# Kernel optimization log

Hardware: AMD Instinct MI355X
Metric: run time of the kernel (lower is better)

## Reference

```python
import jax, jax.numpy as jnp
import numpy as np

B, IN_CH, N, DIM, PH, HID, K = 4, 128, 2048, 256, 64, 1024, 16
EPS = 1e-5


def conv1(x, w, b):
    # 1x1 Conv1d: x (B,C,N), w (O,C) -> (B,O,N)
    return jnp.einsum('oc,bcn->bon', w, x) + b[None, :, None]


def conv2(x, w, b):
    # 1x1 Conv2d: x (B,C,N,K), w (O,C) -> (B,O,N,K)
    return jnp.einsum('oc,bcnk->bonk', w, x) + b[None, :, None, None]


def bn2(x, g, beta, mean, var):
    # eval-mode BatchNorm2d over channel dim of (B,C,N,K)
    scale = g * jax.lax.rsqrt(var + EPS)
    return x * scale[None, :, None, None] + (beta - mean * scale)[None, :, None, None]


def query_knn(pos, k):
    # pos: (B,3,N). Returns (B,N,K) indices of k nearest neighbors (incl. self).
    p = jnp.transpose(pos, (0, 2, 1))                     # (B,N,3)
    sq = jnp.sum(p * p, axis=-1)                          # (B,N)
    dist = sq[:, :, None] + sq[:, None, :] - 2.0 * jnp.einsum('bnc,bmc->bnm', p, p)
    _, idx = jax.lax.top_k(-dist, k)                      # smallest distances first
    return idx


def group(feat, idx):
    # feat: (B,C,N), idx: (B,N,K) -> (B,C,N,K) where out[b,c,i,k]=feat[b,c,idx[b,i,k]]
    b, c, n = feat.shape
    k = idx.shape[-1]
    ib = jnp.broadcast_to(idx.reshape(b, 1, n * k), (b, c, n * k))
    return jnp.take_along_axis(feat, ib, axis=2).reshape(b, c, n, k)


def setup_inputs() -> dict:
    key = jax.random.key(0)
    ks = jax.random.split(key, 12)
    s = 0.02
    return {
        'x': jax.random.normal(ks[0], (B, IN_CH, N), jnp.float32),
        'pos': jax.random.normal(ks[1], (B, 3, N), jnp.float32),
        'ls_w': jax.random.normal(ks[2], (DIM, IN_CH), jnp.float32) * s,
        'ls_b': jnp.zeros((DIM,), jnp.float32),
        'kw': jax.random.normal(ks[3], (DIM, DIM), jnp.float32) * s,
        'kb': jnp.zeros((DIM,), jnp.float32),
        'qw': jax.random.normal(ks[4], (DIM, DIM), jnp.float32) * s,
        'qb': jnp.zeros((DIM,), jnp.float32),
        'vw': jax.random.normal(ks[5], (DIM, DIM), jnp.float32) * s,
        'vb': jnp.zeros((DIM,), jnp.float32),
        'pw1': jax.random.normal(ks[6], (PH, 3), jnp.float32) * s,
        'pb1': jnp.zeros((PH,), jnp.float32),
        'pg': jnp.ones((PH,), jnp.float32),
        'pbeta': jnp.zeros((PH,), jnp.float32),
        'pmean': jnp.zeros((PH,), jnp.float32),
        'pvar': jnp.ones((PH,), jnp.float32),
        'pw2': jax.random.normal(ks[7], (DIM, PH), jnp.float32) * s,
        'pb2': jnp.zeros((DIM,), jnp.float32),
        'aw1': jax.random.normal(ks[8], (HID, DIM), jnp.float32) * s,
        'ab1': jnp.zeros((HID,), jnp.float32),
        'ag': jnp.ones((HID,), jnp.float32),
        'abeta': jnp.zeros((HID,), jnp.float32),
        'amean': jnp.zeros((HID,), jnp.float32),
        'avar': jnp.ones((HID,), jnp.float32),
        'aw2': jax.random.normal(ks[9], (DIM, HID), jnp.float32) * s,
        'ab2': jnp.zeros((DIM,), jnp.float32),
        'lw': jax.random.normal(ks[10], (IN_CH, DIM), jnp.float32) * s,
        'lb': jnp.zeros((IN_CH,), jnp.float32),
    }


def reference(x, pos, ls_w, ls_b, kw, kb, qw, qb, vw, vb,
              pw1, pb1, pg, pbeta, pmean, pvar, pw2, pb2,
              aw1, ab1, ag, abeta, amean, avar, aw2, ab2, lw, lb):
    identity = x
    h = conv1(x, ls_w, ls_b)                              # (B,DIM,N)
    idx = query_knn(pos, K)                               # (B,N,K) int32
    key_f = group(conv1(h, kw, kb), idx)                  # (B,DIM,N,K)
    value = conv1(h, vw, vb)                              # (B,DIM,N)
    query = conv1(h, qw, qb)                              # (B,DIM,N)
    qk_rel = query[:, :, :, None] - key_f                 # (B,DIM,N,K)
    pos_rel = pos[:, :, :, None] - group(pos, idx)        # (B,3,N,K)
    pe = conv2(jax.nn.relu(bn2(conv2(pos_rel, pw1, pb1), pg, pbeta, pmean, pvar)), pw2, pb2)
    attn = conv2(jax.nn.relu(bn2(conv2(qk_rel + pe, aw1, ab1), ag, abeta, amean, avar)), aw2, ab2)
    attn = jax.nn.softmax(attn, axis=-1)                  # softmax over K
    val_g = group(value, idx) + pe                        # (B,DIM,N,K)
    agg = jnp.sum(attn * val_g, axis=-1)                  # (B,DIM,N)
    y = conv1(agg, lw, lb)                                # (B,IN_CH,N)
    return y + identity
```

## Files before the change

### kernel.cpp

```cpp
#include <hip/hip_runtime.h>
#include <hip/hip_bf16.h>
#include <math.h>

#define B_    4
#define CIN   128
#define NPTS  2048
#define DIM   256
#define PH    64
#define HIDN  1024
#define KNN_  16
#define BN    (B_*NPTS)
#define CC    (BN*KNN_)
#define EPS_  1e-5f

typedef __bf16 bf16;
typedef __bf16 bf16x8 __attribute__((ext_vector_type(8)));
typedef __bf16 bf16x4 __attribute__((ext_vector_type(4)));
typedef float  f32x4  __attribute__((ext_vector_type(4)));

__global__ __launch_bounds__(256) void prep_kernel(
    const float* __restrict__ ls_w, const float* __restrict__ kw,
    const float* __restrict__ qw,   const float* __restrict__ vw,
    const float* __restrict__ pw2,  const float* __restrict__ aw1,
    const float* __restrict__ aw2,  const float* __restrict__ lw,
    const float* __restrict__ pb1,  const float* __restrict__ pg,
    const float* __restrict__ pbeta,const float* __restrict__ pmean,
    const float* __restrict__ pvar,
    const float* __restrict__ ab1,  const float* __restrict__ ag,
    const float* __restrict__ abeta,const float* __restrict__ amean,
    const float* __restrict__ avar,
    const float* __restrict__ qb,   const float* __restrict__ kb,
    const float* __restrict__ vb,
    bf16* ls_wb, bf16* qkvw, bf16* pw2b, bf16* aw1b, bf16* aw2b, bf16* lwb,
    float* pe_scale, float* pe_shift, float* at_scale, float* at_shift,
    float* qkvb)
{
  long e = (long)blockIdx.x * 256 + threadIdx.x;
  if (e < 32768)  { ls_wb[e] = (bf16)ls_w[e]; return; } e -= 32768;
  if (e < 65536)  { qkvw[e]          = (bf16)qw[e]; return; } e -= 65536;
  if (e < 65536)  { qkvw[65536 + e]  = (bf16)kw[e]; return; } e -= 65536;
  if (e < 65536)  { qkvw[131072 + e] = (bf16)vw[e]; return; } e -= 65536;
  if (e < 16384)  { pw2b[e]  = (bf16)pw2[e];  return; } e -= 16384;
  if (e < 262144) { aw1b[e]  = (bf16)aw1[e];  return; } e -= 262144;
  if (e < 262144) { aw2b[e]  = (bf16)aw2[e];  return; } e -= 262144;
  if (e < 32768)  { lwb[e]   = (bf16)lw[e];   return; } e -= 32768;
  if (e < 64) {
    float sc = pg[e] * rsqrtf(pvar[e] + EPS_);
    pe_scale[e] = sc;
    pe_shift[e] = sc * pb1[e] + pbeta[e] - pmean[e] * sc;
    return;
  } e -= 64;
  if (e < 1024) {
    float sc = ag[e] * rsqrtf(avar[e] + EPS_);
    at_scale[e] = sc;
    at_shift[e] = sc * ab1[e] + abeta[e] - amean[e] * sc;
    return;
  } e -= 1024;
  if (e < 768) {
    qkvb[e] = (e < 256) ? qb[e] : (e < 512) ? kb[e - 256] : vb[e - 512];
  }
}

__global__ __launch_bounds__(256) void transpose_x_kernel(
    const float* __restrict__ x, bf16* __restrict__ xT)
{
  __shared__ float tile[CIN][65];
  const int tid = threadIdx.x;
  const int b = blockIdx.x >> 5;
  const int n0 = (blockIdx.x & 31) * 64;
  const float* xb = x + (long)b * CIN * NPTS;
#pragma unroll
  for (int it = 0; it < 32; ++it) {
    int row = it * 4 + (tid >> 6);
    int n = tid & 63;
    tile[row][n] = xb[(long)row * NPTS + n0 + n];
  }
  __syncthreads();
#pragma unroll
  for (int it = 0; it < 4; ++it) {
    int c = it * 256 + tid;
    int n = c >> 4;
    int ch0 = (c & 15) * 8;
    bf16x8 v;
#pragma unroll
    for (int j = 0; j < 8; ++j) v[j] = (bf16)tile[ch0 + j][n];
    *(bf16x8*)&xT[((long)b * NPTS + n0 + n) * CIN + ch0] = v;
  }
}

__global__ __launch_bounds__(256) void knn_kernel(
    const float* __restrict__ pos, int* __restrict__ idx_out)
{
  __shared__ float px[NPTS], py[NPTS], pz[NPTS];
  const int tid = threadIdx.x;
  const int lane = tid & 63, wave = tid >> 6;
  const int q = blockIdx.x * 4 + wave;
  const int b = q >> 11;
  const int n = q & (NPTS - 1);
  const float* p = pos + (long)b * 3 * NPTS;
  for (int j = tid; j < NPTS; j += 256) {
    px[j] = p[j]; py[j] = p[NPTS + j]; pz[j] = p[2 * NPTS + j];
  }
  __syncthreads();
  float qx = px[n], qy = py[n], qz = pz[n];
  float qs = qx * qx + qy * qy + qz * qz;
  float d[32];
#pragma unroll
  for (int j = 0; j < 32; ++j) {
    int pt = j * 64 + lane;
    float x = px[pt], y = py[pt], z = pz[pt];
    float s2 = x * x + y * y + z * z;
    float dt = qx * x + qy * y + qz * z;
    d[j] = qs + s2 - 2.f * dt;
  }
  for (int r = 0; r < KNN_; ++r) {
    float bv = 1e30f; int bj = 0;
#pragma unroll
    for (int j = 0; j < 32; ++j)
      if (d[j] < bv) { bv = d[j]; bj = j; }
    int bi = bj * 64 + lane;
#pragma unroll
    for (int off = 32; off >= 1; off >>= 1) {
      float ov = __shfl_xor(bv, off);
      int   oi = __shfl_xor(bi, off);
      if (ov < bv || (ov == bv && oi < bi)) { bv = ov; bi = oi; }
    }
    if (lane == 0) idx_out[(long)q * KNN_ + r] = bi;
#pragma unroll
    for (int j = 0; j < 32; ++j)
      if (bi == j * 64 + lane) d[j] = 1e30f;
  }
}

template<int KD, bool OBF16>
__global__ __launch_bounds__(256) void gemmT_kernel(
    const bf16* __restrict__ inT, const bf16* __restrict__ Wb,
    const float* __restrict__ bias, void* __restrict__ outp, int O)
{
  const int tid = threadIdx.x;
  const int lane = tid & 63, wave = tid >> 6;
  const int row16 = lane & 15, grp = lane >> 4;
  const long i0 = (long)blockIdx.x * 64 + (wave & 1) * 32;
  const long o0 = (long)blockIdx.y * 64 + (wave >> 1) * 32;
  f32x4 acc[2][2] = {};
  const bf16* a0p = inT + (i0 + row16) * KD + grp * 8;
  const bf16* a1p = a0p + 16 * KD;
  const bf16* b0p = Wb + (o0 + row16) * KD + grp * 8;
  const bf16* b1p = b0p + 16 * KD;
#pragma unroll
  for (int ks = 0; ks < KD / 32; ++ks) {
    bf16x8 a0 = *(const bf16x8*)(a0p + ks * 32);
    bf16x8 a1 = *(const bf16x8*)(a1p + ks * 32);
    bf16x8 b0 = *(const bf16x8*)(b0p + ks * 32);
    bf16x8 b1 = *(const bf16x8*)(b1p + ks * 32);
    acc[0][0] = __builtin_amdgcn_mfma_f32_16x16x32_bf16(a0, b0, acc[0][0], 0, 0, 0);
    acc[0][1] = __builtin_amdgcn_mfma_f32_16x16x32_bf16(a0, b1, acc[0][1], 0, 0, 0);
    acc[1][0] = __builtin_amdgcn_mfma_f32_16x16x32_bf16(a1, b0, acc[1][0], 0, 0, 0);
    acc[1][1] = __builtin_amdgcn_mfma_f32_16x16x32_bf16(a1, b1, acc[1][1], 0, 0, 0);
  }
#pragma unroll
  for (int ot = 0; ot < 2; ++ot) {
    long o = o0 + ot * 16 + row16;
    float bv = bias[o];
#pragma unroll
    for (int it = 0; it < 2; ++it) {
#pragma unroll
      for (int r = 0; r < 4; ++r) {
        long i = i0 + it * 16 + grp * 4 + r;
        float v = acc[it][ot][r] + bv;
        if (OBF16) ((bf16*)outp)[i * O + o] = (bf16)v;
        else       ((float*)outp)[i * O + o] = v;
      }
    }
  }
}

__global__ __launch_bounds__(512, 4) void attn_fused_kernel(
    const bf16* __restrict__ qkvT, const float* __restrict__ pos,
    const int* __restrict__ idx, const float* __restrict__ pw1,
    const float* __restrict__ pe_scale, const float* __restrict__ pe_shift,
    const bf16* __restrict__ pw2b, const float* __restrict__ pb2,
    const bf16* __restrict__ aw1b, const bf16* __restrict__ aw2b,
    const float* __restrict__ at_scale, const float* __restrict__ at_shift,
    const float* __restrict__ ab2, bf16* __restrict__ aggT)
{
  __shared__ __align__(16) bf16 u_lds[64][264];
  __shared__ __align__(16) bf16 tbuf[64 * 136];
  __shared__ float rel_lds[64][4];
  __shared__ int   idx_lds[64];
  bf16 (*t_lds)[136]  = (bf16(*)[136])tbuf;
  bf16 (*hid_lds)[72] = (bf16(*)[72])tbuf;

  const int tid = threadIdx.x;
  const int lane = tid & 63, wave = tid >> 6;
  const int row16 = lane & 15, grp = lane >> 4;
  const long c0 = (long)blockIdx.x * 64;
  const int bn0 = blockIdx.x * 4;
  const int b = bn0 >> 11;
  const float* pB = pos + (long)b * 3 * NPTS;
  const int os = wave * 32;

  if (tid < 64) {
    int nb = idx[c0 + tid];
    idx_lds[tid] = nb;
    int n = (bn0 + (tid >> 4)) & (NPTS - 1);
    rel_lds[tid][0] = pB[n] - pB[nb];
    rel_lds[tid][1] = pB[NPTS + n] - pB[NPTS + nb];
    rel_lds[tid][2] = pB[2 * NPTS + n] - pB[2 * NPTS + nb];
  }
#pragma unroll
  for (int it = 0; it < 4; ++it) {
    int id = it * 512 + tid;
    int col = id >> 5, ch16 = id & 31;
    int nb = idx[c0 + col];
    *(bf16x8*)&u_lds[col][ch16 * 8] =
        *(const bf16x8*)(qkvT + ((long)b * NPTS + nb) * 768 + 256 + ch16 * 8);
  }
  __syncthreads();

  {
    int c = tid & 63, jq = tid >> 6;
    float rx = rel_lds[c][0], ry = rel_lds[c][1], rz = rel_lds[c][2];
#pragma unroll
    for (int jj = 0; jj < 8; ++jj) {
      int j = jq * 8 + jj;
      float v = pw1[j * 3] * rx + pw1[j * 3 + 1] * ry + pw1[j * 3 + 2] * rz;
      v = pe_scale[j] * v + pe_shift[j];
      hid_lds[c][j] = (bf16)fmaxf(v, 0.f);
    }
  }
  __syncthreads();

  f32x4 accpe[4][2] = {};
#pragma unroll
  for (int ks = 0; ks < 2; ++ks) {
    bf16x8 ah[4];
#pragma unroll
    for (int ct = 0; ct < 4; ++ct)
      ah[ct] = *(const bf16x8*)&hid_lds[ct * 16 + row16][ks * 32 + grp * 8];
#pragma unroll
    for (int ot = 0; ot < 2; ++ot) {
      bf16x8 bw = *(const bf16x8*)(pw2b + (long)(os + ot * 16 + row16) * PH + ks * 32 + grp * 8);
#pragma unroll
      for (int ct = 0; ct < 4; ++ct)
        accpe[ct][ot] = __builtin_amdgcn_mfma_f32_16x16x32_bf16(ah[ct], bw, accpe[ct][ot], 0, 0, 0);
    }
  }

  bf16x4 pe_bf[4][2];
#pragma unroll
  for (int ot = 0; ot < 2; ++ot) {
    int o = os + ot * 16 + row16;
    float pb2v = pb2[o];
#pragma unroll
    for (int ct = 0; ct < 4; ++ct) {
      float qv = (float)qkvT[(long)(bn0 + ct) * 768 + o];
#pragma unroll
      for (int r = 0; r < 4; ++r) {
        int c = ct * 16 + grp * 4 + r;
        float pev = accpe[ct][ot][r] + pb2v;
        float kv = (float)u_lds[c][o];
        u_lds[c][o] = (bf16)(qv - kv + pev);
        pe_bf[ct][ot][r] = (bf16)pev;
      }
    }
  }
  __syncthreads();

  const int hs = wave * 32;
  const int hs16 = wave * 16;
  f32x4 acc2[4][2] = {};
  for (int jc = 0; jc < 8; ++jc) {
    const int hg = jc * 128 + hs16;
    f32x4 acc1[4] = {};
#pragma unroll
    for (int ks = 0; ks < 8; ++ks) {
      bf16x8 bu[4];
#pragma unroll
      for (int ct = 0; ct < 4; ++ct)
        bu[ct] = *(const bf16x8*)&u_lds[ct * 16 + row16][ks * 32 + grp * 8];
      bf16x8 aw = *(const bf16x8*)(aw1b + (long)(hg + row16) * DIM + ks * 32 + grp * 8);
#pragma unroll
      for (int ct = 0; ct < 4; ++ct)
        acc1[ct] = __builtin_amdgcn_mfma_f32_16x16x32_bf16(aw, bu[ct], acc1[ct], 0, 0, 0);
    }
    {
      f32x4 sc4 = *(const f32x4*)&at_scale[hg + grp * 4];
      f32x4 sh4 = *(const f32x4*)&at_shift[hg + grp * 4];
#pragma unroll
      for (int ct = 0; ct < 4; ++ct) {
        bf16x4 pk;
#pragma unroll
        for (int r = 0; r < 4; ++r) {
          float v = sc4[r] * acc1[ct][r] + sh4[r];
          pk[r] = (bf16)fmaxf(v, 0.f);
        }
        *(bf16x4*)&t_lds[ct * 16 + row16][hs16 + grp * 4] = pk;
      }
    }
    __syncthreads();
#pragma unroll
    for (int ks2 = 0; ks2 < 4; ++ks2) {
      bf16x8 a2[4], b2;
#pragma unroll
      for (int ct = 0; ct < 4; ++ct)
        a2[ct] = *(const bf16x8*)&t_lds[ct * 16 + row16][ks2 * 32 + grp * 8];
#pragma unroll
      for (int ot = 0; ot < 2; ++ot) {
        b2 = *(const bf16x8*)(aw2b + (long)(os + ot * 16 + row16) * HIDN + jc * 128 + ks2 * 32 + grp * 8);
#pragma unroll
        for (int ct = 0; ct < 4; ++ct)
          acc2[ct][ot] = __builtin_amdgcn_mfma_f32_16x16x32_bf16(a2[ct], b2, acc2[ct][ot], 0, 0, 0);
      }
    }
    __syncthreads();
  }

#pragma unroll
  for (int ct = 0; ct < 4; ++ct) {
#pragma unroll
    for (int ot = 0; ot < 2; ++ot) {
      int o = os + ot * 16 + row16;
      float ab = ab2[o];
      float l[4];
      float m = -1e30f;
#pragma unroll
      for (int r = 0; r < 4; ++r) {
        l[r] = acc2[ct][ot][r] + ab;
        m = fmaxf(m, l[r]);
      }
      m = fmaxf(m, __shfl_xor(m, 16));
      m = fmaxf(m, __shfl_xor(m, 32));
      float s = 0.f;
#pragma unroll
      for (int r = 0; r < 4; ++r) { l[r] = __expf(l[r] - m); s += l[r]; }
      s += __shfl_xor(s, 16);
      s += __shfl_xor(s, 32);
      float inv = 1.f / s;
      float agg = 0.f;
#pragma unroll
      for (int r = 0; r < 4; ++r) {
        int c = ct * 16 + grp * 4 + r;
        int nb = idx_lds[c];
        float vv = (float)qkvT[((long)b * NPTS + nb) * 768 + 512 + o];
        agg += l[r] * (vv + (float)pe_bf[ct][ot][r]);
      }
      agg *= inv;
      agg += __shfl_xor(agg, 16);
      agg += __shfl_xor(agg, 32);
      if (grp == 0) aggT[(long)(bn0 + ct) * DIM + o] = (bf16)agg;
    }
  }
}

__global__ __launch_bounds__(256) void final_kernel(
    const bf16* __restrict__ aggT, const bf16* __restrict__ lwb,
    const float* __restrict__ lb, const float* __restrict__ x,
    float* __restrict__ out)
{
  const int tid = threadIdx.x;
  const int lane = tid & 63, wave = tid >> 6;
  const int row16 = lane & 15, grp = lane >> 4;
  const long i0 = (long)blockIdx.x * 64 + (wave & 1) * 32;
  const int o0 = blockIdx.y * 64 + (wave >> 1) * 32;
  f32x4 acc[2][2] = {};
  const bf16* a0p = aggT + (i0 + row16) * DIM + grp * 8;
  const bf16* a1p = a0p + 16 * DIM;
  const bf16* b0p = lwb + (long)(o0 + row16) * DIM + grp * 8;
  const bf16* b1p = b0p + 16 * DIM;
#pragma unroll
  for (int ks = 0; ks < 8; ++ks) {
    bf16x8 a0 = *(const bf16x8*)(a0p + ks * 32);
    bf16x8 a1 = *(const bf16x8*)(a1p + ks * 32);
    bf16x8 b0 = *(const bf16x8*)(b0p + ks * 32);
    bf16x8 b1 = *(const bf16x8*)(b1p + ks * 32);
    acc[0][0] = __builtin_amdgcn_mfma_f32_16x16x32_bf16(a0, b0, acc[0][0], 0, 0, 0);
    acc[0][1] = __builtin_amdgcn_mfma_f32_16x16x32_bf16(a0, b1, acc[0][1], 0, 0, 0);
    acc[1][0] = __builtin_amdgcn_mfma_f32_16x16x32_bf16(a1, b0, acc[1][0], 0, 0, 0);
    acc[1][1] = __builtin_amdgcn_mfma_f32_16x16x32_bf16(a1, b1, acc[1][1], 0, 0, 0);
  }
#pragma unroll
  for (int ot = 0; ot < 2; ++ot) {
    int o = o0 + ot * 16 + row16;
    float bv = lb[o];
#pragma unroll
    for (int it = 0; it < 2; ++it) {
#pragma unroll
      for (int r = 0; r < 4; ++r) {
        long i = i0 + it * 16 + grp * 4 + r;
        int bb = (int)(i >> 11);
        int n = (int)(i & (NPTS - 1));
        long off = ((long)bb * CIN + o) * NPTS + n;
        out[off] = acc[it][ot][r] + bv + x[off];
      }
    }
  }
}

extern "C" void kernel_launch(void* const* d_in, const int* in_sizes, int n_in,
                              void* d_out, int out_size, void* d_ws, size_t ws_size,
                              hipStream_t stream)
{
  const float* x     = (const float*)d_in[0];
  const float* pos   = (const float*)d_in[1];
  const float* ls_w  = (const float*)d_in[2];
  const float* ls_b  = (const float*)d_in[3];
  const float* kw    = (const float*)d_in[4];
  const float* kb    = (const float*)d_in[5];
  const float* qw    = (const float*)d_in[6];
  const float* qb    = (const float*)d_in[7];
  const float* vw    = (const float*)d_in[8];
  const float* vb    = (const float*)d_in[9];
  const float* pw1   = (const float*)d_in[10];
  const float* pb1   = (const float*)d_in[11];
  const float* pg    = (const float*)d_in[12];
  const float* pbeta = (const float*)d_in[13];
  const float* pmean = (const float*)d_in[14];
  const float* pvar  = (const float*)d_in[15];
  const float* pw2   = (const float*)d_in[16];
  const float* pb2   = (const float*)d_in[17];
  const float* aw1   = (const float*)d_in[18];
  const float* ab1   = (const float*)d_in[19];
  const float* ag    = (const float*)d_in[20];
  const float* abeta = (const float*)d_in[21];
  const float* amean = (const float*)d_in[22];
  const float* avar  = (const float*)d_in[23];
  const float* aw2   = (const float*)d_in[24];
  const float* ab2   = (const float*)d_in[25];
  const float* lw    = (const float*)d_in[26];
  const float* lb    = (const float*)d_in[27];

  char* ws = (char*)d_ws;
  size_t off = 0;
  auto alloc = [&](size_t bytes) -> void* {
    void* p = ws + off;
    off = (off + bytes + 255) & ~(size_t)255;
    return p;
  };

  bf16* ls_wb = (bf16*)alloc(32768 * 2);
  bf16* qkvw  = (bf16*)alloc(196608 * 2);
  bf16* pw2b  = (bf16*)alloc(16384 * 2);
  bf16* aw1b  = (bf16*)alloc(262144 * 2);
  bf16* aw2b  = (bf16*)alloc(262144 * 2);
  bf16* lwb   = (bf16*)alloc(32768 * 2);
  float* pe_scale = (float*)alloc(64 * 4);
  float* pe_shift = (float*)alloc(64 * 4);
  float* at_scale = (float*)alloc(1024 * 4);
  float* at_shift = (float*)alloc(1024 * 4);
  float* qkvb = (float*)alloc(768 * 4);
  int*  idx  = (int*)alloc((size_t)CC * 4);
  bf16* xT   = (bf16*)alloc((size_t)BN * CIN * 2);
  bf16* hT   = (bf16*)alloc((size_t)BN * DIM * 2);
  bf16* qkvT = (bf16*)alloc((size_t)BN * 768 * 2);
  bf16* aggT = (bf16*)alloc((size_t)BN * DIM * 2);

  prep_kernel<<<dim3((804672 + 255) / 256), 256, 0, stream>>>(
      ls_w, kw, qw, vw, pw2, aw1, aw2, lw,
      pb1, pg, pbeta, pmean, pvar, ab1, ag, abeta, amean, avar,
      qb, kb, vb,
      ls_wb, qkvw, pw2b, aw1b, aw2b, lwb,
      pe_scale, pe_shift, at_scale, at_shift, qkvb);

  transpose_x_kernel<<<dim3(B_ * 32), 256, 0, stream>>>(x, xT);

  knn_kernel<<<dim3(BN / 4), 256, 0, stream>>>(pos, idx);

  gemmT_kernel<128, true><<<dim3(BN / 64, DIM / 64), 256, 0, stream>>>(xT, ls_wb, ls_b, hT, DIM);

  gemmT_kernel<256, true><<<dim3(BN / 64, 768 / 64), 256, 0, stream>>>(hT, qkvw, qkvb, qkvT, 768);

  attn_fused_kernel<<<dim3(CC / 64), 512, 0, stream>>>(
      qkvT, pos, idx, pw1, pe_scale, pe_shift, pw2b, pb2,
      aw1b, aw2b, at_scale, at_shift, ab2, aggT);

  final_kernel<<<dim3(BN / 64, CIN / 64), 256, 0, stream>>>(aggT, lwb, lb, x, (float*)d_out);
}
```

Measured before the change: 477.9 us.

## XOR-swizzle attention LDS tiles, drop padding, raise occupancy hint

Replaces the padded shared-memory arrays in the fused attention kernel with unpadded buffers using an XOR swizzle on 8-element blocks. The aim is to avoid LDS bank conflicts on the MFMA operand reads while shrinking the LDS footprint. The relative-position scratch now lives inside the reusable tbuf region, and neighbor indices are re-read from global memory instead of LDS. The launch bound's occupancy hint rises from 4 to 6, which tightens the register budget and risks spills.

```diff
diff --git a/kernel.cpp b/kernel.cpp
--- a/kernel.cpp
+++ b/kernel.cpp
@@ -175,7 +175,7 @@
   }
 }
 
-__global__ __launch_bounds__(512, 4) void attn_fused_kernel(
+__global__ __launch_bounds__(512, 6) void attn_fused_kernel(
     const bf16* __restrict__ qkvT, const float* __restrict__ pos,
     const int* __restrict__ idx, const float* __restrict__ pw1,
     const float* __restrict__ pe_scale, const float* __restrict__ pe_shift,
@@ -184,16 +184,16 @@
     const float* __restrict__ at_scale, const float* __restrict__ at_shift,
     const float* __restrict__ ab2, bf16* __restrict__ aggT)
 {
-  __shared__ __align__(16) bf16 u_lds[64][264];
-  __shared__ __align__(16) bf16 tbuf[64 * 136];
-  __shared__ float rel_lds[64][4];
-  __shared__ int   idx_lds[64];
-  bf16 (*t_lds)[136]  = (bf16(*)[136])tbuf;
-  bf16 (*hid_lds)[72] = (bf16(*)[72])tbuf;
+  __shared__ __align__(16) bf16 u_lds[64 * 256];
+  __shared__ __align__(16) bf16 tbuf[64 * 128];
+  bf16* t_lds   = tbuf;
+  bf16* hid_lds = tbuf;
+  float (*rel4)[4] = (float(*)[4])(tbuf + 6144);
 
   const int tid = threadIdx.x;
   const int lane = tid & 63, wave = tid >> 6;
   const int row16 = lane & 15, grp = lane >> 4;
+  const int r7 = row16 & 7;
   const long c0 = (long)blockIdx.x * 64;
   const int bn0 = blockIdx.x * 4;
   const int b = bn0 >> 11;
@@ -202,32 +202,33 @@
 
   if (tid < 64) {
     int nb = idx[c0 + tid];
-    idx_lds[tid] = nb;
     int n = (bn0 + (tid >> 4)) & (NPTS - 1);
-    rel_lds[tid][0] = pB[n] - pB[nb];
-    rel_lds[tid][1] = pB[NPTS + n] - pB[NPTS + nb];
-    rel_lds[tid][2] = pB[2 * NPTS + n] - pB[2 * NPTS + nb];
+    rel4[tid][0] = pB[n] - pB[nb];
+    rel4[tid][1] = pB[NPTS + n] - pB[NPTS + nb];
+    rel4[tid][2] = pB[2 * NPTS + n] - pB[2 * NPTS + nb];
   }
 #pragma unroll
   for (int it = 0; it < 4; ++it) {
     int id = it * 512 + tid;
     int col = id >> 5, ch16 = id & 31;
     int nb = idx[c0 + col];
-    *(bf16x8*)&u_lds[col][ch16 * 8] =
+    *(bf16x8*)&u_lds[col * 256 + ((ch16 ^ (col & 7)) << 3)] =
         *(const bf16x8*)(qkvT + ((long)b * NPTS + nb) * 768 + 256 + ch16 * 8);
   }
   __syncthreads();
 
   {
     int c = tid & 63, jq = tid >> 6;
-    float rx = rel_lds[c][0], ry = rel_lds[c][1], rz = rel_lds[c][2];
+    float rx = rel4[c][0], ry = rel4[c][1], rz = rel4[c][2];
+    bf16x8 pk8;
 #pragma unroll
     for (int jj = 0; jj < 8; ++jj) {
       int j = jq * 8 + jj;
       float v = pw1[j * 3] * rx + pw1[j * 3 + 1] * ry + pw1[j * 3 + 2] * rz;
       v = pe_scale[j] * v + pe_shift[j];
-      hid_lds[c][j] = (bf16)fmaxf(v, 0.f);
-    }
+      pk8[jj] = (bf16)fmaxf(v, 0.f);
+    }
+    *(bf16x8*)&hid_lds[c * 64 + ((jq ^ (c & 7)) << 3)] = pk8;
   }
   __syncthreads();
 
@@ -237,7 +238,7 @@
     bf16x8 ah[4];
 #pragma unroll
     for (int ct = 0; ct < 4; ++ct)
-      ah[ct] = *(const bf16x8*)&hid_lds[ct * 16 + row16][ks * 32 + grp * 8];
+      ah[ct] = *(const bf16x8*)&hid_lds[(ct * 16 + row16) * 64 + (((ks * 4 + grp) ^ r7) << 3)];
 #pragma unroll
     for (int ot = 0; ot < 2; ++ot) {
       bf16x8 bw = *(const bf16x8*)(pw2b + (long)(os + ot * 16 + row16) * PH + ks * 32 + grp * 8);
@@ -258,16 +259,16 @@
 #pragma unroll
       for (int r = 0; r < 4; ++r) {
         int c = ct * 16 + grp * 4 + r;
+        int ua = c * 256 + (((o >> 3) ^ (c & 7)) << 3) + (o & 7);
         float pev = accpe[ct][ot][r] + pb2v;
-        float kv = (float)u_lds[c][o];
-        u_lds[c][o] = (bf16)(qv - kv + pev);
+        float kv = (float)u_lds[ua];
+        u_lds[ua] = (bf16)(qv - kv + pev);
         pe_bf[ct][ot][r] = (bf16)pev;
       }
     }
   }
   __syncthreads();
 
-  const int hs = wave * 32;
   const int hs16 = wave * 16;
   f32x4 acc2[4][2] = {};
   for (int jc = 0; jc < 8; ++jc) {
@@ -276,9 +277,10 @@
 #pragma unroll
     for (int ks = 0; ks < 8; ++ks) {
       bf16x8 bu[4];
+      const int ublk = ((ks * 4 + grp) ^ r7) << 3;
 #pragma unroll
       for (int ct = 0; ct < 4; ++ct)
-        bu[ct] = *(const bf16x8*)&u_lds[ct * 16 + row16][ks * 32 + grp * 8];
+        bu[ct] = *(const bf16x8*)&u_lds[(ct * 16 + row16) * 256 + ublk];
       bf16x8 aw = *(const bf16x8*)(aw1b + (long)(hg + row16) * DIM + ks * 32 + grp * 8);
 #pragma unroll
       for (int ct = 0; ct < 4; ++ct)
@@ -295,7 +297,9 @@
           float v = sc4[r] * acc1[ct][r] + sh4[r];
           pk[r] = (bf16)fmaxf(v, 0.f);
         }
-        *(bf16x4*)&t_lds[ct * 16 + row16][hs16 + grp * 4] = pk;
+        int trow = ct * 16 + row16;
+        int tblk = (wave * 2 + (grp >> 1)) ^ (trow & 7);
+        *(bf16x4*)&t_lds[trow * 128 + (tblk << 3) + ((grp & 1) << 2)] = pk;
       }
     }
     __syncthreads();
@@ -304,7 +308,7 @@
       bf16x8 a2[4], b2;
 #pragma unroll
       for (int ct = 0; ct < 4; ++ct)
-        a2[ct] = *(const bf16x8*)&t_lds[ct * 16 + row16][ks2 * 32 + grp * 8];
+        a2[ct] = *(const bf16x8*)&t_lds[(ct * 16 + row16) * 128 + (((ks2 * 4 + grp) ^ r7) << 3)];
 #pragma unroll
       for (int ot = 0; ot < 2; ++ot) {
         b2 = *(const bf16x8*)(aw2b + (long)(os + ot * 16 + row16) * HIDN + jc * 128 + ks2 * 32 + grp * 8);
@@ -341,7 +345,7 @@
 #pragma unroll
       for (int r = 0; r < 4; ++r) {
         int c = ct * 16 + grp * 4 + r;
-        int nb = idx_lds[c];
+        int nb = idx[c0 + c];
         float vv = (float)qkvT[((long)b * NPTS + nb) * 768 + 512 + o];
         agg += l[r] * (vv + (float)pe_bf[ct][ot][r]);
       }
```

Result: slower. 542.4 us (+13.5%).

## Fold linear-stem conv into QKV weights and merge setup kernels into one launch

Applied to the files above, without the earlier changes.

The 1x1 stem conv (ls_w) is folded algebraically into the Q/K/V projection weights and biases, computed on device, so the QKV GEMM runs directly on the transposed input with K=128. This removes the intermediate h tensor and one GEMM. The prep, transpose, kNN and weight-fold work are combined into a single launch partitioned by block index, which cuts launch count. The folded weights are rounded to bf16 after an fp32 product, which changes numerics slightly, and the fold blocks run a naive serial 256-step loop per output row.

```diff
diff --git a/kernel.cpp b/kernel.cpp
--- a/kernel.cpp
+++ b/kernel.cpp
@@ -18,9 +18,20 @@
 typedef __bf16 bf16x4 __attribute__((ext_vector_type(4)));
 typedef float  f32x4  __attribute__((ext_vector_type(4)));
 
-__global__ __launch_bounds__(256) void prep_kernel(
-    const float* __restrict__ ls_w, const float* __restrict__ kw,
-    const float* __restrict__ qw,   const float* __restrict__ vw,
+#define KNN_END   2048
+#define PREP_CNT  2245
+#define PREP_END  (KNN_END + PREP_CNT)
+#define TR_END    (PREP_END + 128)
+#define FOLD_END  (TR_END + 192)
+
+__global__ __launch_bounds__(256) void combo_kernel(
+    const float* __restrict__ pos, int* __restrict__ idx_out,
+    const float* __restrict__ x, bf16* __restrict__ xT,
+    const float* __restrict__ ls_w, const float* __restrict__ ls_b,
+    const float* __restrict__ qw, const float* __restrict__ kw,
+    const float* __restrict__ vw,
+    const float* __restrict__ qb, const float* __restrict__ kb,
+    const float* __restrict__ vb,
     const float* __restrict__ pw2,  const float* __restrict__ aw1,
     const float* __restrict__ aw2,  const float* __restrict__ lw,
     const float* __restrict__ pb1,  const float* __restrict__ pg,
@@ -29,106 +40,122 @@
     const float* __restrict__ ab1,  const float* __restrict__ ag,
     const float* __restrict__ abeta,const float* __restrict__ amean,
     const float* __restrict__ avar,
-    const float* __restrict__ qb,   const float* __restrict__ kb,
-    const float* __restrict__ vb,
-    bf16* ls_wb, bf16* qkvw, bf16* pw2b, bf16* aw1b, bf16* aw2b, bf16* lwb,
+    bf16* pw2b, bf16* aw1b, bf16* aw2b, bf16* lwb,
     float* pe_scale, float* pe_shift, float* at_scale, float* at_shift,
-    float* qkvb)
+    bf16* wfold, float* bfold)
 {
-  long e = (long)blockIdx.x * 256 + threadIdx.x;
-  if (e < 32768)  { ls_wb[e] = (bf16)ls_w[e]; return; } e -= 32768;
-  if (e < 65536)  { qkvw[e]          = (bf16)qw[e]; return; } e -= 65536;
-  if (e < 65536)  { qkvw[65536 + e]  = (bf16)kw[e]; return; } e -= 65536;
-  if (e < 65536)  { qkvw[131072 + e] = (bf16)vw[e]; return; } e -= 65536;
-  if (e < 16384)  { pw2b[e]  = (bf16)pw2[e];  return; } e -= 16384;
-  if (e < 262144) { aw1b[e]  = (bf16)aw1[e];  return; } e -= 262144;
-  if (e < 262144) { aw2b[e]  = (bf16)aw2[e];  return; } e -= 262144;
-  if (e < 32768)  { lwb[e]   = (bf16)lw[e];   return; } e -= 32768;
-  if (e < 64) {
-    float sc = pg[e] * rsqrtf(pvar[e] + EPS_);
-    pe_scale[e] = sc;
-    pe_shift[e] = sc * pb1[e] + pbeta[e] - pmean[e] * sc;
+  __shared__ __align__(16) char smem[33280];
+  const int bid = blockIdx.x;
+  const int tid = threadIdx.x;
+
+  if (bid < KNN_END) {
+    float* px = (float*)smem;
+    float* py = px + NPTS;
+    float* pz = py + NPTS;
+    const int lane = tid & 63, wave = tid >> 6;
+    const int q = bid * 4 + wave;
+    const int b = q >> 11;
+    const int n = q & (NPTS - 1);
+    const float* p = pos + (long)b * 3 * NPTS;
+    for (int j = tid; j < NPTS; j += 256) {
+      px[j] = p[j]; py[j] = p[NPTS + j]; pz[j] = p[2 * NPTS + j];
+    }
+    __syncthreads();
+    float qx = px[n], qy = py[n], qz = pz[n];
+    float qs = qx * qx + qy * qy + qz * qz;
+    float d[32];
+#pragma unroll
+    for (int j = 0; j < 32; ++j) {
+      int pt = j * 64 + lane;
+      float xx = px[pt], yy = py[pt], zz = pz[pt];
+      float s2 = xx * xx + yy * yy + zz * zz;
+      float dt = qx * xx + qy * yy + qz * zz;
+      d[j] = qs + s2 - 2.f * dt;
+    }
+    for (int r = 0; r < KNN_; ++r) {
+      float bv = 1e30f; int bj = 0;
+#pragma unroll
+      for (int j = 0; j < 32; ++j)
+        if (d[j] < bv) { bv = d[j]; bj = j; }
+      int bi = bj * 64 + lane;
+#pragma unroll
+      for (int off = 32; off >= 1; off >>= 1) {
+        float ov = __shfl_xor(bv, off);
+        int   oi = __shfl_xor(bi, off);
+        if (ov < bv || (ov == bv && oi < bi)) { bv = ov; bi = oi; }
+      }
+      if (lane == 0) idx_out[(long)q * KNN_ + r] = bi;
+#pragma unroll
+      for (int j = 0; j < 32; ++j)
+        if (bi == j * 64 + lane) d[j] = 1e30f;
+    }
     return;
-  } e -= 64;
-  if (e < 1024) {
-    float sc = ag[e] * rsqrtf(avar[e] + EPS_);
-    at_scale[e] = sc;
-    at_shift[e] = sc * ab1[e] + abeta[e] - amean[e] * sc;
+  }
+
+  if (bid < PREP_END) {
+    long e = (long)(bid - KNN_END) * 256 + tid;
+    if (e < 16384)  { pw2b[e] = (bf16)pw2[e]; return; } e -= 16384;
+    if (e < 262144) { aw1b[e] = (bf16)aw1[e]; return; } e -= 262144;
+    if (e < 262144) { aw2b[e] = (bf16)aw2[e]; return; } e -= 262144;
+    if (e < 32768)  { lwb[e]  = (bf16)lw[e];  return; } e -= 32768;
+    if (e < 64) {
+      float sc = pg[e] * rsqrtf(pvar[e] + EPS_);
+      pe_scale[e] = sc;
+      pe_shift[e] = sc * pb1[e] + pbeta[e] - pmean[e] * sc;
+      return;
+    } e -= 64;
+    if (e < 1024) {
+      float sc = ag[e] * rsqrtf(avar[e] + EPS_);
+      at_scale[e] = sc;
+      at_shift[e] = sc * ab1[e] + abeta[e] - amean[e] * sc;
+    }
     return;
-  } e -= 1024;
-  if (e < 768) {
-    qkvb[e] = (e < 256) ? qb[e] : (e < 512) ? kb[e - 256] : vb[e - 512];
-  }
-}
-
-__global__ __launch_bounds__(256) void transpose_x_kernel(
-    const float* __restrict__ x, bf16* __restrict__ xT)
-{
-  __shared__ float tile[CIN][65];
-  const int tid = threadIdx.x;
-  const int b = blockIdx.x >> 5;
-  const int n0 = (blockIdx.x & 31) * 64;
-  const float* xb = x + (long)b * CIN * NPTS;
-#pragma unroll
-  for (int it = 0; it < 32; ++it) {
-    int row = it * 4 + (tid >> 6);
-    int n = tid & 63;
-    tile[row][n] = xb[(long)row * NPTS + n0 + n];
-  }
-  __syncthreads();
-#pragma unroll
-  for (int it = 0; it < 4; ++it) {
-    int c = it * 256 + tid;
-    int n = c >> 4;
-    int ch0 = (c & 15) * 8;
-    bf16x8 v;
-#pragma unroll
-    for (int j = 0; j < 8; ++j) v[j] = (bf16)tile[ch0 + j][n];
-    *(bf16x8*)&xT[((long)b * NPTS + n0 + n) * CIN + ch0] = v;
-  }
-}
-
-__global__ __launch_bounds__(256) void knn_kernel(
-    const float* __restrict__ pos, int* __restrict__ idx_out)
-{
-  __shared__ float px[NPTS], py[NPTS], pz[NPTS];
-  const int tid = threadIdx.x;
-  const int lane = tid & 63, wave = tid >> 6;
-  const int q = blockIdx.x * 4 + wave;
-  const int b = q >> 11;
-  const int n = q & (NPTS - 1);
-  const float* p = pos + (long)b * 3 * NPTS;
-  for (int j = tid; j < NPTS; j += 256) {
-    px[j] = p[j]; py[j] = p[NPTS + j]; pz[j] = p[2 * NPTS + j];
-  }
-  __syncthreads();
-  float qx = px[n], qy = py[n], qz = pz[n];
-  float qs = qx * qx + qy * qy + qz * qz;
-  float d[32];
-#pragma unroll
-  for (int j = 0; j < 32; ++j) {
-    int pt = j * 64 + lane;
-    float x = px[pt], y = py[pt], z = pz[pt];
-    float s2 = x * x + y * y + z * z;
-    float dt = qx * x + qy * y + qz * z;
-    d[j] = qs + s2 - 2.f * dt;
-  }
-  for (int r = 0; r < KNN_; ++r) {
-    float bv = 1e30f; int bj = 0;
-#pragma unroll
-    for (int j = 0; j < 32; ++j)
-      if (d[j] < bv) { bv = d[j]; bj = j; }
-    int bi = bj * 64 + lane;
-#pragma unroll
-    for (int off = 32; off >= 1; off >>= 1) {
-      float ov = __shfl_xor(bv, off);
-      int   oi = __shfl_xor(bi, off);
-      if (ov < bv || (ov == bv && oi < bi)) { bv = ov; bi = oi; }
-    }
-    if (lane == 0) idx_out[(long)q * KNN_ + r] = bi;
-#pragma unroll
-    for (int j = 0; j < 32; ++j)
-      if (bi == j * 64 + lane) d[j] = 1e30f;
+  }
+
+  if (bid < TR_END) {
+    float (*tile)[65] = (float(*)[65])smem;
+    const int tb = bid - PREP_END;
+    const int b = tb >> 5;
+    const int n0 = (tb & 31) * 64;
+    const float* xb = x + (long)b * CIN * NPTS;
+#pragma unroll
+    for (int it = 0; it < 32; ++it) {
+      int row = it * 4 + (tid >> 6);
+      int n = tid & 63;
+      tile[row][n] = xb[(long)row * NPTS + n0 + n];
+    }
+    __syncthreads();
+#pragma unroll
+    for (int it = 0; it < 4; ++it) {
+      int c = it * 256 + tid;
+      int n = c >> 4;
+      int ch0 = (c & 15) * 8;
+      bf16x8 v;
+#pragma unroll
+      for (int j = 0; j < 8; ++j) v[j] = (bf16)tile[ch0 + j][n];
+      *(bf16x8*)&xT[((long)b * NPTS + n0 + n) * CIN + ch0] = v;
+    }
+    return;
+  }
+
+  {
+    const int lane = tid & 63, wave = tid >> 6;
+    const int o = (bid - TR_END) * 4 + wave;
+    const float* wsrc; const float* bsrc; int oo;
+    if (o < 256)      { wsrc = qw + (long)o * DIM;        bsrc = qb; oo = o; }
+    else if (o < 512) { wsrc = kw + (long)(o - 256) * DIM; bsrc = kb; oo = o - 256; }
+    else              { wsrc = vw + (long)(o - 512) * DIM; bsrc = vb; oo = o - 512; }
+    const int c0 = lane, c1 = lane + 64;
+    float acc0 = 0.f, acc1 = 0.f, accb = 0.f;
+    for (int dd = 0; dd < DIM; ++dd) {
+      float w = wsrc[dd];
+      acc0 += w * ls_w[(long)dd * CIN + c0];
+      acc1 += w * ls_w[(long)dd * CIN + c1];
+      accb += w * ls_b[dd];
+    }
+    wfold[(long)o * CIN + c0] = (bf16)acc0;
+    wfold[(long)o * CIN + c1] = (bf16)acc1;
+    if (lane == 0) bfold[o] = accb + bsrc[oo];
   }
 }
 
@@ -267,7 +294,6 @@
   }
   __syncthreads();
 
-  const int hs = wave * 32;
   const int hs16 = wave * 16;
   f32x4 acc2[4][2] = {};
   for (int jc = 0; jc < 8; ++jc) {
@@ -438,8 +464,6 @@
     return p;
   };
 
-  bf16* ls_wb = (bf16*)alloc(32768 * 2);
-  bf16* qkvw  = (bf16*)alloc(196608 * 2);
   bf16* pw2b  = (bf16*)alloc(16384 * 2);
   bf16* aw1b  = (bf16*)alloc(262144 * 2);
   bf16* aw2b  = (bf16*)alloc(262144 * 2);
@@ -448,27 +472,23 @@
   float* pe_shift = (float*)alloc(64 * 4);
   float* at_scale = (float*)alloc(1024 * 4);
   float* at_shift = (float*)alloc(1024 * 4);
-  float* qkvb = (float*)alloc(768 * 4);
+  bf16* wfold = (bf16*)alloc(98304 * 2);
+  float* bfold = (float*)alloc(768 * 4);
   int*  idx  = (int*)alloc((size_t)CC * 4);
   bf16* xT   = (bf16*)alloc((size_t)BN * CIN * 2);
-  bf16* hT   = (bf16*)alloc((size_t)BN * DIM * 2);
   bf16* qkvT = (bf16*)alloc((size_t)BN * 768 * 2);
   bf16* aggT = (bf16*)alloc((size_t)BN * DIM * 2);
 
-  prep_kernel<<<dim3((804672 + 255) / 256), 256, 0, stream>>>(
-      ls_w, kw, qw, vw, pw2, aw1, aw2, lw,
+  combo_kernel<<<dim3(FOLD_END), 256, 0, stream>>>(
+      pos, idx, x, xT,
+      ls_w, ls_b, qw, kw, vw, qb, kb, vb,
+      pw2, aw1, aw2, lw,
       pb1, pg, pbeta, pmean, pvar, ab1, ag, abeta, amean, avar,
-      qb, kb, vb,
-      ls_wb, qkvw, pw2b, aw1b, aw2b, lwb,
-      pe_scale, pe_shift, at_scale, at_shift, qkvb);
-
-  transpose_x_kernel<<<dim3(B_ * 32), 256, 0, stream>>>(x, xT);
-
-  knn_kernel<<<dim3(BN / 4), 256, 0, stream>>>(pos, idx);
-
-  gemmT_kernel<128, true><<<dim3(BN / 64, DIM / 64), 256, 0, stream>>>(xT, ls_wb, ls_b, hT, DIM);
-
-  gemmT_kernel<256, true><<<dim3(BN / 64, 768 / 64), 256, 0, stream>>>(hT, qkvw, qkvb, qkvT, 768);
+      pw2b, aw1b, aw2b, lwb,
+      pe_scale, pe_shift, at_scale, at_shift,
+      wfold, bfold);
+
+  gemmT_kernel<128, true><<<dim3(BN / 64, 768 / 64), 256, 0, stream>>>(xT, wfold, bfold, qkvT, 768);
 
   attn_fused_kernel<<<dim3(CC / 64), 512, 0, stream>>>(
       qkvT, pos, idx, pw1, pe_scale, pe_shift, pw2b, pb2,
```

New measurement: 464.4 us. -2.8%, faster.
